# Kernel tuning notes

Measured on AMD Instinct MI355X. Metric: run time of the kernel, lower is better.

The kernel has to match this reference:

```python
import jax, jax.numpy as jnp
import numpy as np

N_NODES = 100000
N_EDGES = 1600000
F_IN, F_HID, F_OUT = 64, 64, 32


def setup_inputs() -> dict:
    key = jax.random.key(0)
    k1, k2, k3, k4 = jax.random.split(key, 4)
    x = jax.random.normal(k1, (N_NODES, F_IN), dtype=jnp.float32)
    edge_idx = jax.random.randint(k2, (2, N_EDGES), 0, N_NODES, dtype=jnp.int64)
    W1 = jax.random.normal(k3, (F_IN, F_HID), dtype=jnp.float32) * (1.0 / np.sqrt(F_IN))
    b1 = jnp.zeros((F_HID,), dtype=jnp.float32)
    W2 = jax.random.normal(k4, (F_HID, F_OUT), dtype=jnp.float32) * (1.0 / np.sqrt(F_HID))
    b2 = jnp.zeros((F_OUT,), dtype=jnp.float32)
    return {"x": x, "edge_idx": edge_idx, "W1": W1, "b1": b1, "W2": W2, "b2": b2}


def _gcn_conv(h, src, dst, norm, W, b, n):
    # PyG GCNConv: transform first, then normalized sum aggregation, then bias.
    h = h @ W                                   # [N, F_out]
    msg = h[src] * norm[:, None]                # [E+N, F_out] gather + scale
    agg = jax.ops.segment_sum(msg, dst, num_segments=n)  # scatter-add
    return agg + b


def reference(x, edge_idx, W1, b1, W2, b2):
    n = x.shape[0]
    loop = jnp.arange(n, dtype=edge_idx.dtype)
    src = jnp.concatenate([edge_idx[0], loop])  # add self-loops
    dst = jnp.concatenate([edge_idx[1], loop])
    # symmetric normalization D^-1/2 (A+I) D^-1/2
    deg = jax.ops.segment_sum(jnp.ones_like(dst, dtype=x.dtype), dst, num_segments=n)
    dinv = jnp.where(deg > 0, jax.lax.rsqrt(deg), 0.0)
    norm = dinv[src] * dinv[dst]                # [E+N]

    h = _gcn_conv(x, src, dst, norm, W1, b1, n)
    h = jax.nn.relu(h)
    # dropout(p=0.5) is identity in eval mode (deterministic reference)
    out = _gcn_conv(h, src, dst, norm, W2, b2, n)
    return out
```

## Files before the change

### kernel.cpp

```cpp
#include <hip/hip_runtime.h>
#include <hip/hip_bf16.h>
#include <hip/hip_fp16.h>


#define N_FEAT_IN 64
#define B2SHIFT 9
#define CHUNK 4096

struct alignas(8) half4 { __half2 lo, hi; };

__global__ __launch_bounds__(1024) void passA_hist(const int* __restrict__ dst,
                                                   int* __restrict__ H, int E) {
    __shared__ int h[256];
    int t = threadIdx.x;
    if (t < 256) h[t] = 0;
    __syncthreads();
    int base = blockIdx.x * CHUNK;
    int end = min(base + CHUNK, E);
    for (int i = base + t; i < end; i += 1024)
        atomicAdd(&h[dst[i] >> B2SHIFT], 1);
    __syncthreads();
    if (t < 256) H[blockIdx.x * 256 + t] = h[t];
}

__global__ __launch_bounds__(512) void col_scan_a(int* __restrict__ H,
                                                  int* __restrict__ ctot, int NR) {
    __shared__ int s[512];
    int b = blockIdx.x;
    int t = threadIdx.x;
    int v = (t < NR) ? H[t * 256 + b] : 0;
    s[t] = v;
    __syncthreads();
    for (int off = 1; off < 512; off <<= 1) {
        int a = (t >= off) ? s[t - off] : 0;
        __syncthreads();
        s[t] += a;
        __syncthreads();
    }
    if (t < NR) H[t * 256 + b] = s[t] - v;
    if (t == 511) ctot[b] = s[511];
}

__global__ __launch_bounds__(256) void col_scan_b(const int* __restrict__ ctot,
                                                  int* __restrict__ cbase,
                                                  int* __restrict__ bbase,
                                                  int* __restrict__ row_ptr,
                                                  int NB, int n, int E) {
    __shared__ int s[256];
    int t = threadIdx.x;
    int v = ctot[t];
    s[t] = v;
    __syncthreads();
    for (int off = 1; off < 256; off <<= 1) {
        int a = (t >= off) ? s[t - off] : 0;
        __syncthreads();
        s[t] += a;
        __syncthreads();
    }
    int e = s[t] - v;
    cbase[t] = e;
    if (t < NB) bbase[t] = e;
    if (t == 0) { bbase[NB] = E; row_ptr[n] = E; }
}

__global__ __launch_bounds__(1024) void passB_place(const int* __restrict__ src,
                                                    const int* __restrict__ dst,
                                                    const int* __restrict__ H,
                                                    const int* __restrict__ cbase,
                                                    unsigned* __restrict__ bedges, int E) {
    __shared__ int cur[256];
    int t = threadIdx.x;
    if (t < 256) cur[t] = H[blockIdx.x * 256 + t] + cbase[t];
    __syncthreads();
    int base = blockIdx.x * CHUNK;
    int end = min(base + CHUNK, E);
    for (int i = base + t; i < end; i += 1024) {
        int d = dst[i];
        int p = atomicAdd(&cur[d >> B2SHIFT], 1);
        bedges[p] = ((unsigned)src[i] << B2SHIFT) | (unsigned)(d & 511);
    }
}

__global__ __launch_bounds__(1024) void bucket_csr(const int* __restrict__ bbase,
                                                   const unsigned* __restrict__ bedges,
                                                   int* __restrict__ row_ptr,
                                                   float* __restrict__ dinv,
                                                   int* __restrict__ csr_src, int n) {
    __shared__ int lh[512];
    __shared__ int cur[512];
    int t = threadIdx.x;
    if (t < 512) lh[t] = 0;
    __syncthreads();
    int b = blockIdx.x;
    int beg = bbase[b], end = bbase[b + 1];
    for (int i = beg + t; i < end; i += 1024)
        atomicAdd(&lh[bedges[i] & 511], 1);
    __syncthreads();
    int c = (t < 512) ? lh[t] : 0;
    for (int off = 1; off < 512; off <<= 1) {
        int a = (t < 512 && t >= off) ? lh[t - off] : 0;
        __syncthreads();
        if (t < 512) lh[t] += a;
        __syncthreads();
    }
    if (t < 512) {
        int d = (b << B2SHIFT) + t;
        int excl = beg + lh[t] - c;
        cur[t] = excl;
        if (d < n) {
            row_ptr[d] = excl;
            dinv[d] = rsqrtf((float)c + 1.0f);
        }
    }
    __syncthreads();
    for (int i = beg + t; i < end; i += 1024) {
        unsigned v = bedges[i];
        int p = atomicAdd(&cur[v & 511], 1);
        csr_src[p] = (int)(v >> B2SHIFT);
    }
}

__global__ __launch_bounds__(256) void gemm64(const float* __restrict__ A,
                                              const float* __restrict__ W,
                                              const float* __restrict__ dinv,
                                              __half* __restrict__ outh, int n) {
    constexpr int K = 64, FO = 64, CPT = 16;
    __shared__ float As[64][K + 4];
    __shared__ float Ws[K][FO];

    const int t = threadIdx.x;
    const int r0 = blockIdx.x * 64;

    if (blockIdx.x == 0 && t < FO)
        outh[(size_t)n * FO + t] = __float2half(0.f);

    for (int i = t; i < K * FO / 4; i += 256) {
        int k = i / (FO / 4);
        int c4 = (i % (FO / 4)) * 4;
        *(float4*)&Ws[k][c4] = *(const float4*)&W[k * FO + c4];
    }
    for (int i = t; i < 1024; i += 256) {
        int row = i / 16;
        int c4 = (i % 16) * 4;
        int g = r0 + row;
        float4 v = make_float4(0.f, 0.f, 0.f, 0.f);
        if (g < n) v = *(const float4*)&A[(size_t)g * K + c4];
        *(float4*)&As[row][c4] = v;
    }
    __syncthreads();

    const int row = t >> 2;
    const int c0 = (t & 3) * CPT;
    float acc[CPT];
#pragma unroll
    for (int j = 0; j < CPT; ++j) acc[j] = 0.f;
#pragma unroll
    for (int k = 0; k < K; ++k) {
        float xv = As[row][k];
#pragma unroll
        for (int j = 0; j < CPT; ++j) acc[j] = fmaf(xv, Ws[k][c0 + j], acc[j]);
    }

    int g = r0 + row;
    if (g < n) {
        float sc = dinv[g];
#pragma unroll
        for (int j4 = 0; j4 < CPT; j4 += 4) {
            half4 h;
            h.lo = __floats2half2_rn(acc[j4] * sc, acc[j4 + 1] * sc);
            h.hi = __floats2half2_rn(acc[j4 + 2] * sc, acc[j4 + 3] * sc);
            *(half4*)&outh[(size_t)g * FO + c0 + j4] = h;
        }
    }
}

__global__ __launch_bounds__(256) void agg64(const int* __restrict__ row_ptr,
                                             const int* __restrict__ csr_src,
                                             const float* __restrict__ dinv,
                                             const __half* __restrict__ xs1,
                                             const float* __restrict__ b1,
                                             __half* __restrict__ th, int n) {
    int d = blockIdx.x * 16 + (threadIdx.x >> 4);
    if (d >= n) return;
    int c = threadIdx.x & 15;

    int beg = row_ptr[d];
    int end = row_ptr[d + 1];

    half4 sv = *(const half4*)&xs1[(size_t)d * 64 + 4 * c];
    float2 slo = __half22float2(sv.lo), shi = __half22float2(sv.hi);
    float a0 = slo.x, a1 = slo.y, a2 = shi.x, a3 = shi.y;

    for (int jb = beg; jb < end; jb += 8) {
        int idx[8];
#pragma unroll
        for (int k = 0; k < 8; ++k) {
            int j = jb + k;
            int s = csr_src[min(j, end - 1)];
            idx[k] = (j < end) ? s : n;
        }
        half4 v[8];
#pragma unroll
        for (int k = 0; k < 8; ++k)
            v[k] = *(const half4*)&xs1[(size_t)idx[k] * 64 + 4 * c];
#pragma unroll
        for (int k = 0; k < 8; ++k) {
            float2 lo = __half22float2(v[k].lo), hi = __half22float2(v[k].hi);
            a0 += lo.x; a1 += lo.y; a2 += hi.x; a3 += hi.y;
        }
    }

    float di = dinv[d];
    float4 bv = *(const float4*)&b1[4 * c];
    float t0 = fmaxf(fmaf(di, a0, bv.x), 0.f);
    float t1 = fmaxf(fmaf(di, a1, bv.y), 0.f);
    float t2 = fmaxf(fmaf(di, a2, bv.z), 0.f);
    float t3 = fmaxf(fmaf(di, a3, bv.w), 0.f);
    half4 h;
    h.lo = __floats2half2_rn(t0, t1);
    h.hi = __floats2half2_rn(t2, t3);
    *(half4*)&th[(size_t)d * 64 + 4 * c] = h;
}

__global__ __launch_bounds__(256) void gemm32h(const __half* __restrict__ Ah,
                                               const float* __restrict__ W,
                                               const float* __restrict__ dinv,
                                               __half* __restrict__ outh, int n) {
    constexpr int K = 64, FO = 32, CPT = 8;
    __shared__ float As[64][K + 4];
    __shared__ float Ws[K][FO];

    const int t = threadIdx.x;
    const int r0 = blockIdx.x * 64;

    if (blockIdx.x == 0 && t < FO)
        outh[(size_t)n * FO + t] = __float2half(0.f);

    for (int i = t; i < K * FO / 4; i += 256) {
        int k = i / (FO / 4);
        int c4 = (i % (FO / 4)) * 4;
        *(float4*)&Ws[k][c4] = *(const float4*)&W[k * FO + c4];
    }
    for (int i = t; i < 1024; i += 256) {
        int row = i / 16;
        int c4 = (i % 16) * 4;
        int g = r0 + row;
        float4 v = make_float4(0.f, 0.f, 0.f, 0.f);
        if (g < n) {
            half4 hv = *(const half4*)&Ah[(size_t)g * K + c4];
            float2 lo = __half22float2(hv.lo), hi = __half22float2(hv.hi);
            v = make_float4(lo.x, lo.y, hi.x, hi.y);
        }
        *(float4*)&As[row][c4] = v;
    }
    __syncthreads();

    const int row = t >> 2;
    const int c0 = (t & 3) * CPT;
    float acc[CPT];
#pragma unroll
    for (int j = 0; j < CPT; ++j) acc[j] = 0.f;
#pragma unroll
    for (int k = 0; k < K; ++k) {
        float xv = As[row][k];
#pragma unroll
        for (int j = 0; j < CPT; ++j) acc[j] = fmaf(xv, Ws[k][c0 + j], acc[j]);
    }

    int g = r0 + row;
    if (g < n) {
        float sc = dinv[g];
#pragma unroll
        for (int j4 = 0; j4 < CPT; j4 += 4) {
            half4 h;
            h.lo = __floats2half2_rn(acc[j4] * sc, acc[j4 + 1] * sc);
            h.hi = __floats2half2_rn(acc[j4 + 2] * sc, acc[j4 + 3] * sc);
            *(half4*)&outh[(size_t)g * FO + c0 + j4] = h;
        }
    }
}

__global__ __launch_bounds__(256) void agg32(const int* __restrict__ row_ptr,
                                             const int* __restrict__ csr_src,
                                             const float* __restrict__ dinv,
                                             const __half* __restrict__ xs2,
                                             const float* __restrict__ b2,
                                             float* __restrict__ out, int n) {
    int d = blockIdx.x * 32 + (threadIdx.x >> 3);
    if (d >= n) return;
    int c = threadIdx.x & 7;

    int beg = row_ptr[d];
    int end = row_ptr[d + 1];

    half4 sv = *(const half4*)&xs2[(size_t)d * 32 + 4 * c];
    float2 slo = __half22float2(sv.lo), shi = __half22float2(sv.hi);
    float a0 = slo.x, a1 = slo.y, a2 = shi.x, a3 = shi.y;

    for (int jb = beg; jb < end; jb += 8) {
        int idx[8];
#pragma unroll
        for (int k = 0; k < 8; ++k) {
            int j = jb + k;
            int s = csr_src[min(j, end - 1)];
            idx[k] = (j < end) ? s : n;
        }
        half4 v[8];
#pragma unroll
        for (int k = 0; k < 8; ++k)
            v[k] = *(const half4*)&xs2[(size_t)idx[k] * 32 + 4 * c];
#pragma unroll
        for (int k = 0; k < 8; ++k) {
            float2 lo = __half22float2(v[k].lo), hi = __half22float2(v[k].hi);
            a0 += lo.x; a1 += lo.y; a2 += hi.x; a3 += hi.y;
        }
    }

    float di = dinv[d];
    float4 bv = *(const float4*)&b2[4 * c];
    float4 r;
    r.x = fmaf(di, a0, bv.x);
    r.y = fmaf(di, a1, bv.y);
    r.z = fmaf(di, a2, bv.z);
    r.w = fmaf(di, a3, bv.w);
    *(float4*)&out[(size_t)d * 32 + 4 * c] = r;
}

extern "C" void kernel_launch(void* const* d_in, const int* in_sizes, int n_in,
                              void* d_out, int out_size, void* d_ws, size_t ws_size,
                              hipStream_t stream) {
    const float* x  = (const float*)d_in[0];
    const int*   ei = (const int*)d_in[1];
    const float* W1 = (const float*)d_in[2];
    const float* b1 = (const float*)d_in[3];
    const float* W2 = (const float*)d_in[4];
    const float* b2 = (const float*)d_in[5];
    float* out = (float*)d_out;

    const int n = in_sizes[0] / N_FEAT_IN;
    const int E = in_sizes[1] / 2;
    const int* srcI = ei;
    const int* dstI = ei + E;

    const int NB = (n + 511) >> B2SHIFT;
    const int NR = (E + CHUNK - 1) / CHUNK;

    char* ws = (char*)d_ws;
    size_t off = 0;
    auto alloc = [&](size_t bytes) {
        void* p = ws + off;
        off += (bytes + 255) & ~(size_t)255;
        return p;
    };
    float*    dinv    = (float*)alloc((size_t)n * 4);
    int*      row_ptr = (int*)alloc((size_t)(n + 1) * 4);
    int*      bbase   = (int*)alloc((size_t)(NB + 1) * 4);
    int*      ctot    = (int*)alloc((size_t)256 * 4);
    int*      cbase   = (int*)alloc((size_t)256 * 4);
    int*      H       = (int*)alloc((size_t)NR * 256 * 4);
    unsigned* bedges  = (unsigned*)alloc((size_t)E * 4);
    int*      csr_src = (int*)alloc((size_t)E * 4);
    __half*   xs1     = (__half*)alloc((size_t)(n + 1) * 64 * 2);
    __half*   th      = (__half*)alloc((size_t)n * 64 * 2);
    __half*   xs2     = (__half*)alloc((size_t)(n + 1) * 32 * 2);

    passA_hist<<<NR, 1024, 0, stream>>>(dstI, H, E);
    col_scan_a<<<256, 512, 0, stream>>>(H, ctot, NR);
    col_scan_b<<<1, 256, 0, stream>>>(ctot, cbase, bbase, row_ptr, NB, n, E);
    passB_place<<<NR, 1024, 0, stream>>>(srcI, dstI, H, cbase, bedges, E);

    bucket_csr<<<NB, 1024, 0, stream>>>(bbase, bedges, row_ptr, dinv, csr_src, n);

    gemm64<<<(n + 63) / 64, 256, 0, stream>>>(x, W1, dinv, xs1, n);

    agg64<<<(n + 15) / 16, 256, 0, stream>>>(row_ptr, csr_src, dinv, xs1, b1, th, n);

    gemm32h<<<(n + 63) / 64, 256, 0, stream>>>(th, W2, dinv, xs2, n);

    agg32<<<(n + 31) / 32, 256, 0, stream>>>(row_ptr, csr_src, dinv, xs2, b2, out, n);
}
```

Baseline: 202.7 us.

## Sort nodes by degree for balanced aggregation and privatize shared histograms

Adds a counting-sort pass over node degrees to build a permutation ordering nodes by descending in-degree, which the two aggregation kernels then use to pick their destination node. This aims to reduce intra-wavefront load imbalance in the edge loops. It also splits the shared-memory histograms in the bucketing kernels into per-subgroup copies to reduce atomic contention. The cost is four extra kernel launches, an extra indirection, and scattered output row writes.

```diff
diff --git a/kernel.cpp b/kernel.cpp
--- a/kernel.cpp
+++ b/kernel.cpp
@@ -6,21 +6,23 @@
 #define N_FEAT_IN 64
 #define B2SHIFT 9
 #define CHUNK 4096
+#define DCHUNK 1024
 
 struct alignas(8) half4 { __half2 lo, hi; };
 
 __global__ __launch_bounds__(1024) void passA_hist(const int* __restrict__ dst,
                                                    int* __restrict__ H, int E) {
-    __shared__ int h[256];
-    int t = threadIdx.x;
-    if (t < 256) h[t] = 0;
-    __syncthreads();
+    __shared__ int h[4][256];
+    int t = threadIdx.x;
+    ((int*)h)[t] = 0;
+    __syncthreads();
+    int sub = (t >> 6) & 3;
     int base = blockIdx.x * CHUNK;
     int end = min(base + CHUNK, E);
     for (int i = base + t; i < end; i += 1024)
-        atomicAdd(&h[dst[i] >> B2SHIFT], 1);
-    __syncthreads();
-    if (t < 256) H[blockIdx.x * 256 + t] = h[t];
+        atomicAdd(&h[sub][dst[i] >> B2SHIFT], 1);
+    __syncthreads();
+    if (t < 256) H[blockIdx.x * 256 + t] = h[0][t] + h[1][t] + h[2][t] + h[3][t];
 }
 
 __global__ __launch_bounds__(512) void col_scan_a(int* __restrict__ H,
@@ -86,26 +88,29 @@
                                                    int* __restrict__ row_ptr,
                                                    float* __restrict__ dinv,
                                                    int* __restrict__ csr_src, int n) {
-    __shared__ int lh[512];
+    __shared__ int lh[2][512];
     __shared__ int cur[512];
     int t = threadIdx.x;
-    if (t < 512) lh[t] = 0;
-    __syncthreads();
+    if (t < 512) { lh[0][t] = 0; lh[1][t] = 0; }
+    __syncthreads();
+    int sub = (t >> 6) & 1;
     int b = blockIdx.x;
     int beg = bbase[b], end = bbase[b + 1];
     for (int i = beg + t; i < end; i += 1024)
-        atomicAdd(&lh[bedges[i] & 511], 1);
-    __syncthreads();
-    int c = (t < 512) ? lh[t] : 0;
+        atomicAdd(&lh[sub][bedges[i] & 511], 1);
+    __syncthreads();
+    if (t < 512) lh[0][t] += lh[1][t];
+    __syncthreads();
+    int c = (t < 512) ? lh[0][t] : 0;
     for (int off = 1; off < 512; off <<= 1) {
-        int a = (t < 512 && t >= off) ? lh[t - off] : 0;
-        __syncthreads();
-        if (t < 512) lh[t] += a;
+        int a = (t < 512 && t >= off) ? lh[0][t - off] : 0;
+        __syncthreads();
+        if (t < 512) lh[0][t] += a;
         __syncthreads();
     }
     if (t < 512) {
         int d = (b << B2SHIFT) + t;
-        int excl = beg + lh[t] - c;
+        int excl = beg + lh[0][t] - c;
         cur[t] = excl;
         if (d < n) {
             row_ptr[d] = excl;
@@ -117,6 +122,73 @@
         unsigned v = bedges[i];
         int p = atomicAdd(&cur[v & 511], 1);
         csr_src[p] = (int)(v >> B2SHIFT);
+    }
+}
+
+__global__ __launch_bounds__(256) void degA(const int* __restrict__ row_ptr,
+                                            int* __restrict__ D, int n) {
+    __shared__ int dh[64];
+    int t = threadIdx.x;
+    if (t < 64) dh[t] = 0;
+    __syncthreads();
+    int base = blockIdx.x * DCHUNK;
+    int end = min(base + DCHUNK, n);
+    for (int d = base + t; d < end; d += 256) {
+        int key = 63 - min(row_ptr[d + 1] - row_ptr[d], 63);
+        atomicAdd(&dh[key], 1);
+    }
+    __syncthreads();
+    if (t < 64) D[blockIdx.x * 64 + t] = dh[t];
+}
+
+__global__ __launch_bounds__(128) void degScanA(int* __restrict__ D,
+                                                int* __restrict__ dtot, int NR2) {
+    __shared__ int s[128];
+    int b = blockIdx.x;
+    int t = threadIdx.x;
+    int v = (t < NR2) ? D[t * 64 + b] : 0;
+    s[t] = v;
+    __syncthreads();
+    for (int off = 1; off < 128; off <<= 1) {
+        int a = (t >= off) ? s[t - off] : 0;
+        __syncthreads();
+        s[t] += a;
+        __syncthreads();
+    }
+    if (t < NR2) D[t * 64 + b] = s[t] - v;
+    if (t == 127) dtot[b] = s[127];
+}
+
+__global__ __launch_bounds__(64) void degScanB(const int* __restrict__ dtot,
+                                               int* __restrict__ dbase) {
+    __shared__ int s[64];
+    int t = threadIdx.x;
+    int v = dtot[t];
+    s[t] = v;
+    __syncthreads();
+    for (int off = 1; off < 64; off <<= 1) {
+        int a = (t >= off) ? s[t - off] : 0;
+        __syncthreads();
+        s[t] += a;
+        __syncthreads();
+    }
+    dbase[t] = s[t] - v;
+}
+
+__global__ __launch_bounds__(256) void degScatter(const int* __restrict__ row_ptr,
+                                                  const int* __restrict__ D,
+                                                  const int* __restrict__ dbase,
+                                                  int* __restrict__ perm, int n) {
+    __shared__ int cur[64];
+    int t = threadIdx.x;
+    if (t < 64) cur[t] = D[blockIdx.x * 64 + t] + dbase[t];
+    __syncthreads();
+    int base = blockIdx.x * DCHUNK;
+    int end = min(base + DCHUNK, n);
+    for (int d = base + t; d < end; d += 256) {
+        int key = 63 - min(row_ptr[d + 1] - row_ptr[d], 63);
+        int pos = atomicAdd(&cur[key], 1);
+        perm[pos] = d;
     }
 }
 
@@ -174,14 +246,16 @@
     }
 }
 
-__global__ __launch_bounds__(256) void agg64(const int* __restrict__ row_ptr,
+__global__ __launch_bounds__(256) void agg64(const int* __restrict__ perm,
+                                             const int* __restrict__ row_ptr,
                                              const int* __restrict__ csr_src,
                                              const float* __restrict__ dinv,
                                              const __half* __restrict__ xs1,
                                              const float* __restrict__ b1,
                                              __half* __restrict__ th, int n) {
-    int d = blockIdx.x * 16 + (threadIdx.x >> 4);
-    if (d >= n) return;
+    int slot = blockIdx.x * 16 + (threadIdx.x >> 4);
+    if (slot >= n) return;
+    int d = perm[slot];
     int c = threadIdx.x & 15;
 
     int beg = row_ptr[d];
@@ -280,14 +354,16 @@
     }
 }
 
-__global__ __launch_bounds__(256) void agg32(const int* __restrict__ row_ptr,
+__global__ __launch_bounds__(256) void agg32(const int* __restrict__ perm,
+                                             const int* __restrict__ row_ptr,
                                              const int* __restrict__ csr_src,
                                              const float* __restrict__ dinv,
                                              const __half* __restrict__ xs2,
                                              const float* __restrict__ b2,
                                              float* __restrict__ out, int n) {
-    int d = blockIdx.x * 32 + (threadIdx.x >> 3);
-    if (d >= n) return;
+    int slot = blockIdx.x * 32 + (threadIdx.x >> 3);
+    if (slot >= n) return;
+    int d = perm[slot];
     int c = threadIdx.x & 7;
 
     int beg = row_ptr[d];
@@ -342,8 +418,9 @@
     const int* srcI = ei;
     const int* dstI = ei + E;
 
-    const int NB = (n + 511) >> B2SHIFT;
-    const int NR = (E + CHUNK - 1) / CHUNK;
+    const int NB  = (n + 511) >> B2SHIFT;
+    const int NR  = (E + CHUNK - 1) / CHUNK;
+    const int NR2 = (n + DCHUNK - 1) / DCHUNK;
 
     char* ws = (char*)d_ws;
     size_t off = 0;
@@ -360,6 +437,10 @@
     int*      H       = (int*)alloc((size_t)NR * 256 * 4);
     unsigned* bedges  = (unsigned*)alloc((size_t)E * 4);
     int*      csr_src = (int*)alloc((size_t)E * 4);
+    int*      D       = (int*)alloc((size_t)NR2 * 64 * 4);
+    int*      dtot    = (int*)alloc((size_t)64 * 4);
+    int*      dbase   = (int*)alloc((size_t)64 * 4);
+    int*      perm    = (int*)alloc((size_t)n * 4);
     __half*   xs1     = (__half*)alloc((size_t)(n + 1) * 64 * 2);
     __half*   th      = (__half*)alloc((size_t)n * 64 * 2);
     __half*   xs2     = (__half*)alloc((size_t)(n + 1) * 32 * 2);
@@ -371,11 +452,16 @@
 
     bucket_csr<<<NB, 1024, 0, stream>>>(bbase, bedges, row_ptr, dinv, csr_src, n);
 
+    degA<<<NR2, 256, 0, stream>>>(row_ptr, D, n);
+    degScanA<<<64, 128, 0, stream>>>(D, dtot, NR2);
+    degScanB<<<1, 64, 0, stream>>>(dtot, dbase);
+    degScatter<<<NR2, 256, 0, stream>>>(row_ptr, D, dbase, perm, n);
+
     gemm64<<<(n + 63) / 64, 256, 0, stream>>>(x, W1, dinv, xs1, n);
 
-    agg64<<<(n + 15) / 16, 256, 0, stream>>>(row_ptr, csr_src, dinv, xs1, b1, th, n);
+    agg64<<<(n + 15) / 16, 256, 0, stream>>>(perm, row_ptr, csr_src, dinv, xs1, b1, th, n);
 
     gemm32h<<<(n + 63) / 64, 256, 0, stream>>>(th, W2, dinv, xs2, n);
 
-    agg32<<<(n + 31) / 32, 256, 0, stream>>>(row_ptr, csr_src, dinv, xs2, b2, out, n);
-}
+    agg32<<<(n + 31) / 32, 256, 0, stream>>>(perm, row_ptr, csr_src, dinv, xs2, b2, out, n);
+}
```

Result: slower. 215.4 us (+6.3%).
